# Kernel optimization log

Measured on AMD Instinct MI355X. Metric: run time of the kernel, lower is better.

## Reference

```python
import jax, jax.numpy as jnp
import numpy as np

SOBEL_X = jnp.array([[-1.0, 0.0, 1.0], [-2.0, 0.0, 2.0], [-1.0, 0.0, 1.0]], dtype=jnp.float32).reshape(1, 1, 3, 3)
SOBEL_Y = jnp.array([[-1.0, -2.0, -1.0], [0.0, 0.0, 0.0], [1.0, 2.0, 1.0]], dtype=jnp.float32).reshape(1, 1, 3, 3)
EPS = 1e-05


def setup_inputs() -> dict:
    key = jax.random.key(0)
    x = jax.random.uniform(key, (32, 1, 1024, 1024), dtype=jnp.float32)
    return {"x": x}


def _conv3x3(x, k):
    # NCHW input, OIHW kernel, stride 1, SAME padding (padding=1 for 3x3)
    return jax.lax.conv_general_dilated(
        x, k, window_strides=(1, 1), padding=((1, 1), (1, 1)),
        dimension_numbers=("NCHW", "OIHW", "NCHW"))


def reference(x) -> jnp.ndarray:
    grad_x = _conv3x3(x, SOBEL_X)
    grad_y = _conv3x3(x, SOBEL_Y)
    return jnp.abs(grad_x) + jnp.abs(grad_y) + EPS
```

## Files before the change

### kernel.cpp

```cpp
#include <hip/hip_runtime.h>
#include <hip/hip_bf16.h>


#define W 1024
#define H 1024
#define EPS 1e-5f

__global__ __launch_bounds__(256) void sobel_kernel(const float* __restrict__ in,
                                                    float* __restrict__ out) {
    const int rowid = blockIdx.x;
    const int img = rowid >> 10;
    const int y = rowid & (H - 1);
    const int x0 = threadIdx.x << 2;

    const size_t img_off = (size_t)img * W * H;
    const float* rm = in + img_off + (size_t)y * W;

    float4 mv = *(const float4*)(rm + x0);
    float ml = (x0 > 0) ? rm[x0 - 1] : 0.0f;
    float mr = (x0 + 4 < W) ? rm[x0 + 4] : 0.0f;

    float4 tv = make_float4(0.f, 0.f, 0.f, 0.f);
    float tl = 0.f, tr = 0.f;
    if (y > 0) {
        const float* rt = rm - W;
        tv = *(const float4*)(rt + x0);
        tl = (x0 > 0) ? rt[x0 - 1] : 0.0f;
        tr = (x0 + 4 < W) ? rt[x0 + 4] : 0.0f;
    }

    float4 bv = make_float4(0.f, 0.f, 0.f, 0.f);
    float bl = 0.f, br = 0.f;
    if (y < H - 1) {
        const float* rb = rm + W;
        bv = *(const float4*)(rb + x0);
        bl = (x0 > 0) ? rb[x0 - 1] : 0.0f;
        br = (x0 + 4 < W) ? rb[x0 + 4] : 0.0f;
    }

    const float T[6] = {tl, tv.x, tv.y, tv.z, tv.w, tr};
    const float M[6] = {ml, mv.x, mv.y, mv.z, mv.w, mr};
    const float B[6] = {bl, bv.x, bv.y, bv.z, bv.w, br};

    float4 o;
    float* op = &o.x;
#pragma unroll
    for (int i = 0; i < 4; ++i) {
        float gx = (T[i + 2] - T[i]) + 2.0f * (M[i + 2] - M[i]) + (B[i + 2] - B[i]);
        float gy = (B[i] + 2.0f * B[i + 1] + B[i + 2]) - (T[i] + 2.0f * T[i + 1] + T[i + 2]);
        op[i] = fabsf(gx) + fabsf(gy) + EPS;
    }

    *(float4*)(out + img_off + (size_t)y * W + x0) = o;
}

extern "C" void kernel_launch(void* const* d_in, const int* in_sizes, int n_in,
                              void* d_out, int out_size, void* d_ws, size_t ws_size,
                              hipStream_t stream) {
    const float* x = (const float*)d_in[0];
    float* out = (float*)d_out;
    const int N = 32;
    dim3 grid(N * H);
    dim3 block(256);
    sobel_kernel<<<grid, block, 0, stream>>>(x, out);
}
```

Measured before the change: 251.6 us.

## Process 16-row strips per block with rolling register window and nontemporal stores

Each block now walks down a 16-row strip and keeps a rolling three-row window in registers, so each input row is loaded roughly once instead of three times from cache. Blocks are remapped with a swizzle that spreads consecutive block IDs across images and strips, and output uses nontemporal stores to avoid polluting cache. The cost is fewer blocks (1/16 as many), which lowers the amount of parallel memory traffic in flight, and loads inside the loop are serialized per row.

```diff
diff --git a/kernel.cpp b/kernel.cpp
--- a/kernel.cpp
+++ b/kernel.cpp
@@ -4,54 +4,57 @@
 
 #define W 1024
 #define H 1024
+#define R 16
 #define EPS 1e-5f
+
+typedef float v4f __attribute__((ext_vector_type(4)));
+
+__device__ __forceinline__ void loadrow(const float* __restrict__ base, int y,
+                                        int x0, float* dst) {
+    if (y < 0 || y >= H) {
+        dst[0] = dst[1] = dst[2] = dst[3] = dst[4] = dst[5] = 0.f;
+        return;
+    }
+    const float* r = base + (size_t)y * W;
+    v4f v = *(const v4f*)(r + x0);
+    dst[1] = v.x; dst[2] = v.y; dst[3] = v.z; dst[4] = v.w;
+    dst[0] = (x0 > 0) ? r[x0 - 1] : 0.f;
+    dst[5] = (x0 + 4 < W) ? r[x0 + 4] : 0.f;
+}
 
 __global__ __launch_bounds__(256) void sobel_kernel(const float* __restrict__ in,
                                                     float* __restrict__ out) {
-    const int rowid = blockIdx.x;
-    const int img = rowid >> 10;
-    const int y = rowid & (H - 1);
+    const int b = blockIdx.x;
+    const int t = ((b & 255) << 3) | (b >> 8);
+    const int img = t >> 6;
+    const int ty = (t & 63) * R;
     const int x0 = threadIdx.x << 2;
 
-    const size_t img_off = (size_t)img * W * H;
-    const float* rm = in + img_off + (size_t)y * W;
+    const float* base = in + (size_t)img * (W * H);
+    float* obase = out + (size_t)img * (W * H);
 
-    float4 mv = *(const float4*)(rm + x0);
-    float ml = (x0 > 0) ? rm[x0 - 1] : 0.0f;
-    float mr = (x0 + 4 < W) ? rm[x0 + 4] : 0.0f;
+    float T[6], M[6], B[6], Nx[6];
+    loadrow(base, ty - 1, x0, T);
+    loadrow(base, ty,     x0, M);
+    loadrow(base, ty + 1, x0, B);
 
-    float4 tv = make_float4(0.f, 0.f, 0.f, 0.f);
-    float tl = 0.f, tr = 0.f;
-    if (y > 0) {
-        const float* rt = rm - W;
-        tv = *(const float4*)(rt + x0);
-        tl = (x0 > 0) ? rt[x0 - 1] : 0.0f;
-        tr = (x0 + 4 < W) ? rt[x0 + 4] : 0.0f;
+#pragma unroll 4
+    for (int i = 0; i < R; ++i) {
+        const int y = ty + i;
+        loadrow(base, y + 2, x0, Nx);
+
+        v4f o;
+#pragma unroll
+        for (int j = 0; j < 4; ++j) {
+            float gx = (T[j + 2] - T[j]) + 2.0f * (M[j + 2] - M[j]) + (B[j + 2] - B[j]);
+            float gy = (B[j] + 2.0f * B[j + 1] + B[j + 2]) - (T[j] + 2.0f * T[j + 1] + T[j + 2]);
+            o[j] = fabsf(gx) + fabsf(gy) + EPS;
+        }
+        __builtin_nontemporal_store(o, (v4f*)(obase + (size_t)y * W + x0));
+
+#pragma unroll
+        for (int j = 0; j < 6; ++j) { T[j] = M[j]; M[j] = B[j]; B[j] = Nx[j]; }
     }
-
-    float4 bv = make_float4(0.f, 0.f, 0.f, 0.f);
-    float bl = 0.f, br = 0.f;
-    if (y < H - 1) {
-        const float* rb = rm + W;
-        bv = *(const float4*)(rb + x0);
-        bl = (x0 > 0) ? rb[x0 - 1] : 0.0f;
-        br = (x0 + 4 < W) ? rb[x0 + 4] : 0.0f;
-    }
-
-    const float T[6] = {tl, tv.x, tv.y, tv.z, tv.w, tr};
-    const float M[6] = {ml, mv.x, mv.y, mv.z, mv.w, mr};
-    const float B[6] = {bl, bv.x, bv.y, bv.z, bv.w, br};
-
-    float4 o;
-    float* op = &o.x;
-#pragma unroll
-    for (int i = 0; i < 4; ++i) {
-        float gx = (T[i + 2] - T[i]) + 2.0f * (M[i + 2] - M[i]) + (B[i + 2] - B[i]);
-        float gy = (B[i] + 2.0f * B[i + 1] + B[i + 2]) - (T[i] + 2.0f * T[i + 1] + T[i + 2]);
-        op[i] = fabsf(gx) + fabsf(gy) + EPS;
-    }
-
-    *(float4*)(out + img_off + (size_t)y * W + x0) = o;
 }
 
 extern "C" void kernel_launch(void* const* d_in, const int* in_sizes, int n_in,
@@ -60,7 +63,7 @@
     const float* x = (const float*)d_in[0];
     float* out = (float*)d_out;
     const int N = 32;
-    dim3 grid(N * H);
+    dim3 grid(N * (H / R));
     dim3 block(256);
     sobel_kernel<<<grid, block, 0, stream>>>(x, out);
 }
```

New measurement: 237.3 us. 1.06x faster.
